# Optimization experiments

Hardware: AMD Instinct MI355X
Metric: run time of the kernel (lower is better)

The kernel has to match this reference:

```python
import jax, jax.numpy as jnp
import numpy as np

B, S, D, H = 1, 2048, 1024, 16
HD = D // H
S_SLOPE = 10.0      # soft_thres_layer s
C_MASK = -10000.0   # soft_thres_layer c == masked_bias
ALPHA = 0.0         # config.threshold
W_STD = 0.02        # GPT2 init std for weights


def setup_inputs() -> dict:
    key = jax.random.key(0)
    k1, k2, k3 = jax.random.split(key, 3)
    return {
        "hidden_states": jax.random.normal(k1, (B, S, D), dtype=jnp.float32),
        "c_attn_w": jax.random.normal(k2, (D, 3 * D), dtype=jnp.float32) * W_STD,
        "c_attn_b": jnp.zeros((3 * D,), dtype=jnp.float32),
        "c_proj_w": jax.random.normal(k3, (D, D), dtype=jnp.float32) * W_STD,
        "c_proj_b": jnp.zeros((D,), dtype=jnp.float32),
    }


def reference(hidden_states, c_attn_w, c_attn_b, c_proj_w, c_proj_b):
    # Conv1D: x @ w + b (GPT2 convention: weight is [in, out])
    qkv = hidden_states @ c_attn_w + c_attn_b            # [B,S,3D]
    q, k, v = jnp.split(qkv, 3, axis=-1)

    def split_heads(x):
        return x.reshape(B, S, H, HD).transpose(0, 2, 1, 3)  # [B,H,S,hd]

    q, k, v = split_heads(q), split_heads(k), split_heads(v)

    # prun path: NO 1/sqrt(d) scaling (skipped when self.prun is True)
    w = jnp.einsum("bhqd,bhkd->bhqk", q, k)              # [B,H,S,S]

    causal = jnp.tril(jnp.ones((S, S), dtype=bool))[None, None]
    w = jnp.where(causal, w, C_MASK)

    # soft-threshold pruning: smoothly pushes scores below alpha toward c=-10000
    w = C_MASK + (w - C_MASK) * jax.nn.sigmoid(S_SLOPE * (w - ALPHA))

    a = jax.nn.softmax(w, axis=-1)                        # attn_dropout = identity (eval)
    out = jnp.einsum("bhqk,bhkd->bhqd", a, v)             # [B,H,S,hd]
    out = out.transpose(0, 2, 1, 3).reshape(B, S, D)      # merge heads
    return out @ c_proj_w + c_proj_b                      # resid_dropout = identity
```

## Files before the change

kernel.cpp:

```cpp
#include <hip/hip_runtime.h>


#define S_LEN 2048
#define DM    1024
#define NH    16
#define HD    64
#define SLOPE 10.0f
#define CMASK -10000.0f
#define SP    2080

typedef short s16x4 __attribute__((ext_vector_type(4)));
typedef short s16x8 __attribute__((ext_vector_type(8)));
typedef float f32x4 __attribute__((ext_vector_type(4)));

#define MFMA16(a,b,c) __builtin_amdgcn_mfma_f32_16x16x32_bf16(a,b,c,0,0,0)
#define GLDS16(g,l) __builtin_amdgcn_global_load_lds( \
    (const __attribute__((address_space(1))) void*)(g), \
    (__attribute__((address_space(3))) void*)(l), 16, 0, 0)

__device__ __forceinline__ short f2bf(float f){
    unsigned u = __float_as_uint(f);
    u += 0x7fffu + ((u >> 16) & 1u);
    return (short)(u >> 16);
}
__device__ __forceinline__ float bf2f(short x){
    return __uint_as_float(((unsigned)(unsigned short)x) << 16);
}
struct bfpair { short hi, lo; };
__device__ __forceinline__ bfpair split_bf(float x){
    bfpair r; r.hi = f2bf(x);
    r.lo = f2bf(x - bf2f(r.hi));
    return r;
}

template<int ROWS, int THREADS>
__device__ __forceinline__ void stage_tile(const short* gbase, int rstride,
                                           short* lds, int tid){
#pragma unroll
    for (int it = 0; it < ROWS*8/THREADS; ++it){
        int s = it*THREADS + tid;
        int row = s >> 3, grp = s & 7;
        const short* src = gbase + (size_t)row*rstride + ((grp ^ (row & 7)) << 3);
        GLDS16(src, lds + (size_t)s*8);
    }
}
__device__ __forceinline__ s16x8 frag(const short* lds, int row, int kg){
    return *(const s16x8*)&lds[row*64 + ((kg ^ (row & 7)) << 3)];
}

__global__ __launch_bounds__(256)
void gemm_qkv(const short* __restrict__ Ahg, const short* __restrict__ Alg,
              const short* __restrict__ Bhg, const short* __restrict__ Blg,
              const float* __restrict__ bias,
              short* __restrict__ QHh, short* __restrict__ QHl,
              short* __restrict__ KH,  short* __restrict__ Vb)
{
    __shared__ __align__(16) short Ah_s[128*64];
    __shared__ __align__(16) short Bh_s[128*64];
    __shared__ __align__(16) short Al_s[128*64];
    __shared__ __align__(16) short Bl_s[128*64];

    const int tid = threadIdx.x, lane = tid & 63, wid = tid >> 6;
    const int lr = lane & 15, lg = lane >> 4;
    const int brow = blockIdx.y*128, bcol = blockIdx.x*128;
    const int sec = bcol >> 10;
    const int wm = (wid >> 1)*64, wn = (wid & 1)*64;

    f32x4 acc[4][4];
#pragma unroll
    for (int m = 0; m < 4; ++m)
#pragma unroll
        for (int n = 0; n < 4; ++n) acc[m][n] = (f32x4){0.f,0.f,0.f,0.f};

    for (int k0 = 0; k0 < DM; k0 += 64){
        stage_tile<128,256>(Ahg + (size_t)brow*DM + k0, DM, Ah_s, tid);
        stage_tile<128,256>(Bhg + (size_t)bcol*DM + k0, DM, Bh_s, tid);
        if (sec == 0){
            stage_tile<128,256>(Alg + (size_t)brow*DM + k0, DM, Al_s, tid);
            stage_tile<128,256>(Blg + (size_t)bcol*DM + k0, DM, Bl_s, tid);
        }
        __syncthreads();
#pragma unroll
        for (int kc = 0; kc < 2; ++kc){
            s16x8 ah[4], al[4], bh[4], bl[4];
#pragma unroll
            for (int m = 0; m < 4; ++m)
                ah[m] = frag(Ah_s, wm + m*16 + lr, kc*4 + lg);
#pragma unroll
            for (int n = 0; n < 4; ++n)
                bh[n] = frag(Bh_s, wn + n*16 + lr, kc*4 + lg);
            if (sec == 0){
#pragma unroll
                for (int m = 0; m < 4; ++m)
                    al[m] = frag(Al_s, wm + m*16 + lr, kc*4 + lg);
#pragma unroll
                for (int n = 0; n < 4; ++n)
                    bl[n] = frag(Bl_s, wn + n*16 + lr, kc*4 + lg);
            }
#pragma unroll
            for (int m = 0; m < 4; ++m)
#pragma unroll
                for (int n = 0; n < 4; ++n){
                    acc[m][n] = MFMA16(ah[m], bh[n], acc[m][n]);
                    if (sec == 0){
                        acc[m][n] = MFMA16(ah[m], bl[n], acc[m][n]);
                        acc[m][n] = MFMA16(al[m], bh[n], acc[m][n]);
                    }
                }
        }
        __syncthreads();
    }

#pragma unroll
    for (int m = 0; m < 4; ++m)
#pragma unroll
        for (int n = 0; n < 4; ++n){
            int row  = brow + wm + m*16 + lg*4;
            int gcol = bcol + wn + n*16 + lr;
            float bv = bias[gcol];
            int h0 = (gcol & 1023) >> 6, d = gcol & 63;
#pragma unroll
            for (int v = 0; v < 4; ++v){
                float val = acc[m][n][v] + bv;
                if (sec == 0){
                    bfpair p = split_bf(val);
                    size_t o = ((size_t)h0*S_LEN + row + v)*HD + d;
                    QHh[o] = p.hi; QHl[o] = p.lo;
                } else if (sec == 1){
                    KH[((size_t)h0*S_LEN + row + v)*HD + d] = f2bf(val);
                } else {
                    Vb[(size_t)(row + v)*DM + (gcol & 1023)] = f2bf(val);
                }
            }
        }
}

__global__ __launch_bounds__(256)
void gemm_proj(const short* __restrict__ Ahg, const short* __restrict__ Bhg,
               const float* __restrict__ bias, float* __restrict__ C)
{
    __shared__ __align__(16) short Ah_s[128*64];
    __shared__ __align__(16) short Bh_s[128*64];

    const int tid = threadIdx.x, lane = tid & 63, wid = tid >> 6;
    const int lr = lane & 15, lg = lane >> 4;
    const int brow = blockIdx.y*128, bcol = blockIdx.x*128;
    const int wm = (wid >> 1)*64, wn = (wid & 1)*64;

    f32x4 acc[4][4];
#pragma unroll
    for (int m = 0; m < 4; ++m)
#pragma unroll
        for (int n = 0; n < 4; ++n) acc[m][n] = (f32x4){0.f,0.f,0.f,0.f};

    for (int k0 = 0; k0 < DM; k0 += 64){
        stage_tile<128,256>(Ahg + (size_t)brow*DM + k0, DM, Ah_s, tid);
        stage_tile<128,256>(Bhg + (size_t)bcol*DM + k0, DM, Bh_s, tid);
        __syncthreads();
#pragma unroll
        for (int kc = 0; kc < 2; ++kc){
            s16x8 ah[4], bh[4];
#pragma unroll
            for (int m = 0; m < 4; ++m)
                ah[m] = frag(Ah_s, wm + m*16 + lr, kc*4 + lg);
#pragma unroll
            for (int n = 0; n < 4; ++n)
                bh[n] = frag(Bh_s, wn + n*16 + lr, kc*4 + lg);
#pragma unroll
            for (int m = 0; m < 4; ++m)
#pragma unroll
                for (int n = 0; n < 4; ++n)
                    acc[m][n] = MFMA16(ah[m], bh[n], acc[m][n]);
        }
        __syncthreads();
    }

#pragma unroll
    for (int m = 0; m < 4; ++m)
#pragma unroll
        for (int n = 0; n < 4; ++n){
            int row  = brow + wm + m*16 + lg*4;
            int gcol = bcol + wn + n*16 + lr;
            float bv = bias[gcol];
#pragma unroll
            for (int v = 0; v < 4; ++v)
                C[(size_t)(row + v)*DM + gcol] = acc[m][n][v] + bv;
        }
}

__global__ __launch_bounds__(256)
void split_f32(const float* __restrict__ x, short* __restrict__ h,
               short* __restrict__ l, int n4)
{
    int i = blockIdx.x*256 + threadIdx.x;
    if (i >= n4) return;
    float4 v = *(const float4*)&x[(size_t)i*4];
    bfpair a = split_bf(v.x), b = split_bf(v.y), c = split_bf(v.z), d = split_bf(v.w);
    s16x4 hv, lv;
    hv.x = a.hi; hv.y = b.hi; hv.z = c.hi; hv.w = d.hi;
    lv.x = a.lo; lv.y = b.lo; lv.z = c.lo; lv.w = d.lo;
    *(s16x4*)&h[(size_t)i*4] = hv;
    *(s16x4*)&l[(size_t)i*4] = lv;
}

template<bool SPL>
__global__ __launch_bounds__(256)
void wtrans(const float* __restrict__ W, int N, short* __restrict__ Th,
            short* __restrict__ Tl)
{
    __shared__ float t[64][65];
    const int tid = threadIdx.x;
    const int tn = blockIdx.x*64, tk = blockIdx.y*64;
#pragma unroll
    for (int it = 0; it < 4; ++it){
        int idx = tid + it*256;
        int r = idx >> 4, c4 = (idx & 15)*4;
        float4 v = *(const float4*)&W[(size_t)(tk + r)*N + tn + c4];
        t[r][c4] = v.x; t[r][c4+1] = v.y; t[r][c4+2] = v.z; t[r][c4+3] = v.w;
    }
    __syncthreads();
#pragma unroll
    for (int it = 0; it < 4; ++it){
        int idx = tid + it*256;
        int n = idx >> 4, c4 = (idx & 15)*4;
        s16x4 hv, lv;
#pragma unroll
        for (int j = 0; j < 4; ++j){
            bfpair p = split_bf(t[c4+j][n]);
            hv[j] = p.hi; lv[j] = p.lo;
        }
        *(s16x4*)&Th[(size_t)(tn + n)*DM + tk + c4] = hv;
        if (SPL && tn < DM)
            *(s16x4*)&Tl[(size_t)(tn + n)*DM + tk + c4] = lv;
    }
}

__global__ __launch_bounds__(256)
void vtrans(const short* __restrict__ Vb, short* __restrict__ Vt)
{
    __shared__ short t[64][66];
    const int tid = threadIdx.x;
    const int td = blockIdx.x*64, ts = blockIdx.y*64;
#pragma unroll
    for (int it = 0; it < 4; ++it){
        int idx = tid + it*256;
        int r = idx >> 4, c4 = (idx & 15)*4;
        s16x4 v = *(const s16x4*)&Vb[(size_t)(ts + r)*DM + td + c4];
        t[r][c4] = v.x; t[r][c4+1] = v.y; t[r][c4+2] = v.z; t[r][c4+3] = v.w;
    }
    __syncthreads();
#pragma unroll
    for (int it = 0; it < 4; ++it){
        int idx = tid + it*256;
        int n = idx >> 4, c4 = (idx & 15)*4;
        s16x4 o;
#pragma unroll
        for (int j = 0; j < 4; ++j) o[j] = t[c4+j][n];
        *(s16x4*)&Vt[(size_t)(td + n)*SP + ts + c4] = o;
    }
}

__global__ __launch_bounds__(64)
void sv_partial(const short* __restrict__ Vb, float* __restrict__ PB)
{
    int b = blockIdx.x, h = blockIdx.y, d = threadIdx.x;
    float s = 0.f;
#pragma unroll 8
    for (int k = 0; k < 64; ++k)
        s += bf2f(Vb[(size_t)(b*64 + k)*DM + h*HD + d]);
    PB[((size_t)h*32 + b)*64 + d] = s;
}
__global__ __launch_bounds__(64)
void sv_suffix(const float* __restrict__ PB, float* __restrict__ SSV)
{
    int h = blockIdx.x, d = threadIdx.x;
    float s = 0.f;
    SSV[((size_t)h*33 + 32)*64 + d] = 0.f;
    for (int b = 31; b >= 0; --b){
        s += PB[((size_t)h*32 + b)*64 + d];
        SSV[((size_t)h*33 + b)*64 + d] = s;
    }
}

__global__ __launch_bounds__(256)
void attn_fwd(const short* __restrict__ QHh, const short* __restrict__ QHl,
              const short* __restrict__ KH, const short* __restrict__ Vt,
              short* __restrict__ acc0, short* __restrict__ acc1,
              short* __restrict__ acc2, float* __restrict__ ML)
{
    __shared__ __align__(16) short kh_s[64*64];
    __shared__ __align__(16) short vt_s[64*64];
    __shared__ __align__(16) short Ps[4][16*72];

    const int j = blockIdx.x;
    const int h = (j & 7) + 8*((j >> 3) & 1);
    const int t = j >> 4;
    int qst, c;
    if (t < 8)      { qst = t; c = 0; }
    else if (t < 24){ int u = t - 8;  qst = 8  + (u >> 1); c = u & 1; }
    else if (t < 48){ int u = t - 24; qst = 16 + u/3;      c = u - (u/3)*3; }
    else            { int u = t - 48; qst = 24 + (u >> 2); c = u & 3; }
    const int kv0 = c*8;
    const int kv1 = min(kv0 + 8, qst + 1);

    const int tid = threadIdx.x, lane = tid & 63, wid = tid >> 6;
    const int lr = lane & 15, lg = lane >> 4;
    const int qrow = qst*64 + wid*16 + lg*4;

    const short* qbh = QHh + ((size_t)h*S_LEN + qst*64 + wid*16)*HD;
    const short* qbl = QHl + ((size_t)h*S_LEN + qst*64 + wid*16)*HD;
    s16x8 aqh[2], aql[2];
#pragma unroll
    for (int kc = 0; kc < 2; ++kc){
        aqh[kc] = *(const s16x8*)&qbh[lr*HD + kc*32 + lg*8];
        aql[kc] = *(const s16x8*)&qbl[lr*HD + kc*32 + lg*8];
    }

    float m_run[4], l_run[4];
    f32x4 acc_o[4];
#pragma unroll
    for (int v = 0; v < 4; ++v){ m_run[v] = -1e30f; l_run[v] = 0.f; }
#pragma unroll
    for (int n = 0; n < 4; ++n) acc_o[n] = (f32x4){0.f,0.f,0.f,0.f};

    for (int kvb = kv0; kvb < kv1; ++kvb){
        __syncthreads();
        stage_tile<64,256>(KH + ((size_t)h*S_LEN + kvb*64)*HD, HD, kh_s, tid);
        stage_tile<64,256>(Vt + (size_t)(h*HD)*SP + kvb*64, SP, vt_s, tid);
        __syncthreads();

        f32x4 sc[4];
#pragma unroll
        for (int n = 0; n < 4; ++n) sc[n] = (f32x4){0.f,0.f,0.f,0.f};
#pragma unroll
        for (int kc = 0; kc < 2; ++kc)
#pragma unroll
            for (int n = 0; n < 4; ++n){
                s16x8 bkh = frag(kh_s, n*16 + lr, kc*4 + lg);
                sc[n] = MFMA16(aqh[kc], bkh, sc[n]);
                sc[n] = MFMA16(aql[kc], bkh, sc[n]);
            }

        float p[4][4], tmax[4];
#pragma unroll
        for (int v = 0; v < 4; ++v) tmax[v] = -1e30f;
        if (kvb == qst){
#pragma unroll
            for (int n = 0; n < 4; ++n){
                int key = kvb*64 + n*16 + lr;
#pragma unroll
                for (int v = 0; v < 4; ++v){
                    float w;
                    if (key > qrow + v) w = CMASK;
                    else {
                        float sv = sc[n][v];
                        float sig = 1.f / (1.f + __expf(-SLOPE*sv));
                        w = CMASK + (sv - CMASK)*sig;
                    }
                    p[n][v] = w;
                    tmax[v] = fmaxf(tmax[v], w);
                }
            }
        } else {
#pragma unroll
            for (int n = 0; n < 4; ++n)
#pragma unroll
                for (int v = 0; v < 4; ++v){
                    float sv = sc[n][v];
                    float sig = 1.f / (1.f + __expf(-SLOPE*sv));
                    float w = CMASK + (sv - CMASK)*sig;
                    p[n][v] = w;
                    tmax[v] = fmaxf(tmax[v], w);
                }
        }
#pragma unroll
        for (int v = 0; v < 4; ++v)
#pragma unroll
            for (int msk = 1; msk < 16; msk <<= 1)
                tmax[v] = fmaxf(tmax[v], __shfl_xor(tmax[v], msk, 64));

        float scale[4], rsum[4];
#pragma unroll
        for (int v = 0; v < 4; ++v){
            float mn = fmaxf(m_run[v], tmax[v]);
            scale[v] = __expf(m_run[v] - mn);
            m_run[v] = mn;
            rsum[v] = 0.f;
        }
#pragma unroll
        for (int n = 0; n < 4; ++n)
#pragma unroll
            for (int v = 0; v < 4; ++v){
                float e = __expf(p[n][v] - m_run[v]);
                p[n][v] = e;
                rsum[v] += e;
            }
#pragma unroll
        for (int v = 0; v < 4; ++v){
#pragma unroll
            for (int msk = 1; msk < 16; msk <<= 1)
                rsum[v] += __shfl_xor(rsum[v], msk, 64);
            l_run[v] = l_run[v]*scale[v] + rsum[v];
        }
#pragma unroll
        for (int n = 0; n < 4; ++n)
#pragma unroll
            for (int v = 0; v < 4; ++v) acc_o[n][v] *= scale[v];

#pragma unroll
        for (int n = 0; n < 4; ++n)
#pragma unroll
            for (int v = 0; v < 4; ++v)
                Ps[wid][(lg*4 + v)*72 + 16*n + lr] = f2bf(p[n][v]);
        asm volatile("s_waitcnt lgkmcnt(0)" ::: "memory");

        s16x8 pa0 = *(const s16x8*)&Ps[wid][lr*72 + lg*8];
        s16x8 pa1 = *(const s16x8*)&Ps[wid][lr*72 + 32 + lg*8];
#pragma unroll
        for (int n = 0; n < 4; ++n){
            s16x8 bv0 = frag(vt_s, 16*n + lr, lg);
            s16x8 bv1 = frag(vt_s, 16*n + lr, 4 + lg);
            acc_o[n] = MFMA16(pa0, bv0, acc_o[n]);
            acc_o[n] = MFMA16(pa1, bv1, acc_o[n]);
        }
    }

    short* ab = (j < 512) ? acc0 + (size_t)j*4096
              : (j < 768) ? acc1 + (size_t)(j-512)*4096
                          : acc2 + (size_t)(j-768)*4096;
#pragma unroll
    for (int n = 0; n < 4; ++n)
#pragma unroll
        for (int v = 0; v < 4; ++v)
            ab[(wid*16 + lg*4 + v)*64 + 16*n + lr] = f2bf(acc_o[n][v]);
    if (lr == 0){
#pragma unroll
        for (int v = 0; v < 4; ++v){
            ML[((size_t)j*64 + wid*16 + lg*4 + v)*2 + 0] = m_run[v];
            ML[((size_t)j*64 + wid*16 + lg*4 + v)*2 + 1] = l_run[v];
        }
    }
}

__global__ __launch_bounds__(256)
void attn_merge(const short* __restrict__ acc0, const short* __restrict__ acc1,
                const short* __restrict__ acc2, const float* __restrict__ ML,
                const float* __restrict__ SSV, short* __restrict__ O)
{
    const int b = blockIdx.x;
    const int h = b & 15, qst = b >> 4;
    const int d = threadIdx.x & 63, rg = threadIdx.x >> 6;
    const int C = (qst + 8) >> 3;
    const int tbase = (qst < 8)  ? qst
                    : (qst < 16) ? 8  + 2*(qst - 8)
                    : (qst < 24) ? 24 + 3*(qst - 16)
                                 : 48 + 4*(qst - 24);
    const float F = (float)(S_LEN - 64*(qst + 1));
    const float svd = SSV[((size_t)h*33 + (qst + 1))*64 + d];

    for (int i = 0; i < 16; ++i){
        int r = rg + 4*i;
        float M = -1e30f;
        for (int c = 0; c < C; ++c){
            int job = (tbase + c)*16 + h;
            M = fmaxf(M, ML[((size_t)job*64 + r)*2]);
        }
        float num = 0.f, den = 0.f;
        for (int c = 0; c < C; ++c){
            int job = (tbase + c)*16 + h;
            float m = ML[((size_t)job*64 + r)*2];
            float l = ML[((size_t)job*64 + r)*2 + 1];
            const short* ab = (job < 512) ? acc0 + (size_t)job*4096
                            : (job < 768) ? acc1 + (size_t)(job-512)*4096
                                          : acc2 + (size_t)(job-768)*4096;
            float e = __expf(m - M);
            num += e * bf2f(ab[r*64 + d]);
            den += e * l;
        }
        float et = __expf(CMASK - M);
        num += et * svd;
        den += et * F;
        O[(size_t)(qst*64 + r)*DM + h*64 + d] = f2bf(num/den);
    }
}

extern "C" void kernel_launch(void* const* d_in, const int* in_sizes, int n_in,
                              void* d_out, int out_size, void* d_ws, size_t ws_size,
                              hipStream_t stream)
{
    (void)in_sizes; (void)n_in; (void)out_size; (void)ws_size;
    const float* hs   = (const float*)d_in[0];
    const float* wqkv = (const float*)d_in[1];
    const float* bqkv = (const float*)d_in[2];
    const float* wprj = (const float*)d_in[3];
    const float* bprj = (const float*)d_in[4];

    char* p = (char*)d_ws;
    short* Ahg  = (short*)(p + (0ull  << 20));
    short* Alg  = (short*)(p + (4ull  << 20));
    short* WqTh = (short*)(p + (8ull  << 20));
    short* WqTl = (short*)(p + (14ull << 20));
    short* QHh  = (short*)(p + (16ull << 20));
    short* QHl  = (short*)(p + (20ull << 20));
    short* KH   = (short*)(p + (24ull << 20));
    short* Vbg  = (short*)(p + (28ull << 20));
    short* VT   = (short*)(p + (32ull << 20));
    float* PB   = (float*)(p + (38ull << 20));
    float* SSV  = (float*)(p + (38ull << 20) + (256ull << 10));
    float* ML   = (float*)(p + (39ull << 20));
    short* O    = Ahg;
    short* WpT  = WqTh;

    split_f32<<<S_LEN*DM/4/256, 256, 0, stream>>>(hs, Ahg, Alg, S_LEN*DM/4);
    wtrans<true><<<dim3(3*DM/64, DM/64), 256, 0, stream>>>(wqkv, 3*DM, WqTh, WqTl);

    gemm_qkv<<<dim3(24, 16), 256, 0, stream>>>(
        Ahg, Alg, WqTh, WqTl, bqkv, QHh, QHl, KH, Vbg);

    wtrans<false><<<dim3(DM/64, DM/64), 256, 0, stream>>>(wprj, DM, WpT, nullptr);
    vtrans<<<dim3(DM/64, S_LEN/64), 256, 0, stream>>>(Vbg, VT);
    sv_partial<<<dim3(32, NH), 64, 0, stream>>>(Vbg, PB);
    sv_suffix<<<NH, 64, 0, stream>>>(PB, SSV);

    attn_fwd<<<1280, 256, 0, stream>>>(QHh, QHl, KH, VT, Alg, WqTl, Vbg, ML);
    attn_merge<<<512, 256, 0, stream>>>(Alg, WqTl, Vbg, ML, SSV, O);

    gemm_proj<<<dim3(8, 16), 256, 0, stream>>>(O, WpT, bprj, (float*)d_out);
}
```

Before: 181.6 us.

## Fuse prep kernels, fold split-bf16 Q GEMM into K=3072 loop, merge sv_partial into vtrans

Merges the input split and both weight transposes into one prep kernel, so the hi/lo parts sit side by side and the Q-section GEMM becomes a single K=3072 loop instead of three MFMAs per step with a branch. The Q/K/V column blocks are interleaved across blockIdx.x to balance load, and the V column sums are folded into the vtrans kernel, which drops the sv_partial launch. The soft-threshold now uses a cheaper rearranged form that clamps to CMASK below -1.5, and the merge division becomes a fast reciprocal. The workspace layout and the accumulator buffer indexing are reshuffled to match. The clamp and the fast division add small numeric differences.

```diff
diff --git a/kernel.cpp b/kernel.cpp
--- a/kernel.cpp
+++ b/kernel.cpp
@@ -33,6 +33,12 @@
     return r;
 }
 
+__device__ __forceinline__ float softthr(float sv){
+    float E = __expf(-SLOPE*sv);
+    float w = sv - __fdividef((sv - CMASK)*E, 1.f + E);
+    return (sv > -1.5f) ? w : CMASK;
+}
+
 template<int ROWS, int THREADS>
 __device__ __forceinline__ void stage_tile(const short* gbase, int rstride,
                                            short* lds, int tid){
@@ -49,168 +55,33 @@
 }
 
 __global__ __launch_bounds__(256)
-void gemm_qkv(const short* __restrict__ Ahg, const short* __restrict__ Alg,
-              const short* __restrict__ Bhg, const short* __restrict__ Blg,
-              const float* __restrict__ bias,
-              short* __restrict__ QHh, short* __restrict__ QHl,
-              short* __restrict__ KH,  short* __restrict__ Vb)
-{
-    __shared__ __align__(16) short Ah_s[128*64];
-    __shared__ __align__(16) short Bh_s[128*64];
-    __shared__ __align__(16) short Al_s[128*64];
-    __shared__ __align__(16) short Bl_s[128*64];
-
-    const int tid = threadIdx.x, lane = tid & 63, wid = tid >> 6;
-    const int lr = lane & 15, lg = lane >> 4;
-    const int brow = blockIdx.y*128, bcol = blockIdx.x*128;
-    const int sec = bcol >> 10;
-    const int wm = (wid >> 1)*64, wn = (wid & 1)*64;
-
-    f32x4 acc[4][4];
-#pragma unroll
-    for (int m = 0; m < 4; ++m)
-#pragma unroll
-        for (int n = 0; n < 4; ++n) acc[m][n] = (f32x4){0.f,0.f,0.f,0.f};
-
-    for (int k0 = 0; k0 < DM; k0 += 64){
-        stage_tile<128,256>(Ahg + (size_t)brow*DM + k0, DM, Ah_s, tid);
-        stage_tile<128,256>(Bhg + (size_t)bcol*DM + k0, DM, Bh_s, tid);
-        if (sec == 0){
-            stage_tile<128,256>(Alg + (size_t)brow*DM + k0, DM, Al_s, tid);
-            stage_tile<128,256>(Blg + (size_t)bcol*DM + k0, DM, Bl_s, tid);
-        }
-        __syncthreads();
-#pragma unroll
-        for (int kc = 0; kc < 2; ++kc){
-            s16x8 ah[4], al[4], bh[4], bl[4];
-#pragma unroll
-            for (int m = 0; m < 4; ++m)
-                ah[m] = frag(Ah_s, wm + m*16 + lr, kc*4 + lg);
-#pragma unroll
-            for (int n = 0; n < 4; ++n)
-                bh[n] = frag(Bh_s, wn + n*16 + lr, kc*4 + lg);
-            if (sec == 0){
-#pragma unroll
-                for (int m = 0; m < 4; ++m)
-                    al[m] = frag(Al_s, wm + m*16 + lr, kc*4 + lg);
-#pragma unroll
-                for (int n = 0; n < 4; ++n)
-                    bl[n] = frag(Bl_s, wn + n*16 + lr, kc*4 + lg);
-            }
-#pragma unroll
-            for (int m = 0; m < 4; ++m)
-#pragma unroll
-                for (int n = 0; n < 4; ++n){
-                    acc[m][n] = MFMA16(ah[m], bh[n], acc[m][n]);
-                    if (sec == 0){
-                        acc[m][n] = MFMA16(ah[m], bl[n], acc[m][n]);
-                        acc[m][n] = MFMA16(al[m], bh[n], acc[m][n]);
-                    }
-                }
-        }
-        __syncthreads();
-    }
-
-#pragma unroll
-    for (int m = 0; m < 4; ++m)
-#pragma unroll
-        for (int n = 0; n < 4; ++n){
-            int row  = brow + wm + m*16 + lg*4;
-            int gcol = bcol + wn + n*16 + lr;
-            float bv = bias[gcol];
-            int h0 = (gcol & 1023) >> 6, d = gcol & 63;
-#pragma unroll
-            for (int v = 0; v < 4; ++v){
-                float val = acc[m][n][v] + bv;
-                if (sec == 0){
-                    bfpair p = split_bf(val);
-                    size_t o = ((size_t)h0*S_LEN + row + v)*HD + d;
-                    QHh[o] = p.hi; QHl[o] = p.lo;
-                } else if (sec == 1){
-                    KH[((size_t)h0*S_LEN + row + v)*HD + d] = f2bf(val);
-                } else {
-                    Vb[(size_t)(row + v)*DM + (gcol & 1023)] = f2bf(val);
-                }
-            }
-        }
-}
-
-__global__ __launch_bounds__(256)
-void gemm_proj(const short* __restrict__ Ahg, const short* __restrict__ Bhg,
-               const float* __restrict__ bias, float* __restrict__ C)
-{
-    __shared__ __align__(16) short Ah_s[128*64];
-    __shared__ __align__(16) short Bh_s[128*64];
-
-    const int tid = threadIdx.x, lane = tid & 63, wid = tid >> 6;
-    const int lr = lane & 15, lg = lane >> 4;
-    const int brow = blockIdx.y*128, bcol = blockIdx.x*128;
-    const int wm = (wid >> 1)*64, wn = (wid & 1)*64;
-
-    f32x4 acc[4][4];
-#pragma unroll
-    for (int m = 0; m < 4; ++m)
-#pragma unroll
-        for (int n = 0; n < 4; ++n) acc[m][n] = (f32x4){0.f,0.f,0.f,0.f};
-
-    for (int k0 = 0; k0 < DM; k0 += 64){
-        stage_tile<128,256>(Ahg + (size_t)brow*DM + k0, DM, Ah_s, tid);
-        stage_tile<128,256>(Bhg + (size_t)bcol*DM + k0, DM, Bh_s, tid);
-        __syncthreads();
-#pragma unroll
-        for (int kc = 0; kc < 2; ++kc){
-            s16x8 ah[4], bh[4];
-#pragma unroll
-            for (int m = 0; m < 4; ++m)
-                ah[m] = frag(Ah_s, wm + m*16 + lr, kc*4 + lg);
-#pragma unroll
-            for (int n = 0; n < 4; ++n)
-                bh[n] = frag(Bh_s, wn + n*16 + lr, kc*4 + lg);
-#pragma unroll
-            for (int m = 0; m < 4; ++m)
-#pragma unroll
-                for (int n = 0; n < 4; ++n)
-                    acc[m][n] = MFMA16(ah[m], bh[n], acc[m][n]);
-        }
-        __syncthreads();
-    }
-
-#pragma unroll
-    for (int m = 0; m < 4; ++m)
-#pragma unroll
-        for (int n = 0; n < 4; ++n){
-            int row  = brow + wm + m*16 + lg*4;
-            int gcol = bcol + wn + n*16 + lr;
-            float bv = bias[gcol];
-#pragma unroll
-            for (int v = 0; v < 4; ++v)
-                C[(size_t)(row + v)*DM + gcol] = acc[m][n][v] + bv;
-        }
-}
-
-__global__ __launch_bounds__(256)
-void split_f32(const float* __restrict__ x, short* __restrict__ h,
-               short* __restrict__ l, int n4)
-{
-    int i = blockIdx.x*256 + threadIdx.x;
-    if (i >= n4) return;
-    float4 v = *(const float4*)&x[(size_t)i*4];
-    bfpair a = split_bf(v.x), b = split_bf(v.y), c = split_bf(v.z), d = split_bf(v.w);
-    s16x4 hv, lv;
-    hv.x = a.hi; hv.y = b.hi; hv.z = c.hi; hv.w = d.hi;
-    lv.x = a.lo; lv.y = b.lo; lv.z = c.lo; lv.w = d.lo;
-    *(s16x4*)&h[(size_t)i*4] = hv;
-    *(s16x4*)&l[(size_t)i*4] = lv;
-}
-
-template<bool SPL>
-__global__ __launch_bounds__(256)
-void wtrans(const float* __restrict__ W, int N, short* __restrict__ Th,
-            short* __restrict__ Tl)
+void prep(const float* __restrict__ hs, const float* __restrict__ wqkv,
+          const float* __restrict__ wprj, short* __restrict__ Ahl,
+          short* __restrict__ WqT, short* __restrict__ WkvT,
+          short* __restrict__ WpT)
 {
     __shared__ float t[64][65];
-    const int tid = threadIdx.x;
-    const int tn = blockIdx.x*64, tk = blockIdx.y*64;
+    const int bx = blockIdx.x, tid = threadIdx.x;
+
+    if (bx < 2048){
+        int i = bx*256 + tid;
+        int elem = i*4, row = elem >> 10, col = elem & 1023;
+        float4 v = *(const float4*)&hs[(size_t)elem];
+        bfpair a = split_bf(v.x), b = split_bf(v.y), c = split_bf(v.z), d = split_bf(v.w);
+        s16x4 hv, lv;
+        hv.x = a.hi; hv.y = b.hi; hv.z = c.hi; hv.w = d.hi;
+        lv.x = a.lo; lv.y = b.lo; lv.z = c.lo; lv.w = d.lo;
+        *(s16x4*)&Ahl[(size_t)row*2048 + col] = hv;
+        *(s16x4*)&Ahl[(size_t)row*2048 + 1024 + col] = lv;
+        return;
+    }
+
+    const float* W; int N, u;
+    if (bx < 2816){ u = bx - 2048; W = wqkv; N = 3072; }
+    else          { u = bx - 2816; W = wprj; N = 1024; }
+    const int ntiles = N >> 6;
+    const int tn = (u % ntiles)*64, tk = (u / ntiles)*64;
+
 #pragma unroll
     for (int it = 0; it < 4; ++it){
         int idx = tid + it*256;
@@ -229,18 +100,154 @@
             bfpair p = split_bf(t[c4+j][n]);
             hv[j] = p.hi; lv[j] = p.lo;
         }
-        *(s16x4*)&Th[(size_t)(tn + n)*DM + tk + c4] = hv;
-        if (SPL && tn < DM)
-            *(s16x4*)&Tl[(size_t)(tn + n)*DM + tk + c4] = lv;
+        if (bx >= 2816){
+            *(s16x4*)&WpT[(size_t)(tn + n)*1024 + tk + c4] = hv;
+        } else if (tn < 1024){
+            *(s16x4*)&WqT[(size_t)(tn + n)*2048 + tk + c4] = hv;
+            *(s16x4*)&WqT[(size_t)(tn + n)*2048 + 1024 + tk + c4] = lv;
+        } else {
+            *(s16x4*)&WkvT[(size_t)(tn + n - 1024)*1024 + tk + c4] = hv;
+        }
     }
 }
 
 __global__ __launch_bounds__(256)
-void vtrans(const short* __restrict__ Vb, short* __restrict__ Vt)
+void gemm_qkv(const short* __restrict__ Ahl, const short* __restrict__ WqT,
+              const short* __restrict__ WkvT, const float* __restrict__ bias,
+              short* __restrict__ QHh, short* __restrict__ QHl,
+              short* __restrict__ KH,  short* __restrict__ Vb)
+{
+    __shared__ __align__(16) short Ah_s[128*64];
+    __shared__ __align__(16) short Bh_s[128*64];
+
+    const int tid = threadIdx.x, lane = tid & 63, wid = tid >> 6;
+    const int lr = lane & 15, lg = lane >> 4;
+    const int brow = blockIdx.y*128;
+    const int xs = blockIdx.x % 3, xi = blockIdx.x / 3;
+    const int bcol = xs*1024 + xi*128;
+    const bool isQ = (xs == 0);
+    const int KTOT = isQ ? 3072 : 1024;
+    const short* Bbase = isQ ? (WqT + (size_t)bcol*2048)
+                             : (WkvT + (size_t)(bcol - 1024)*1024);
+    const int bstride = isQ ? 2048 : 1024;
+    const int wm = (wid >> 1)*64, wn = (wid & 1)*64;
+
+    f32x4 acc[4][4];
+#pragma unroll
+    for (int m = 0; m < 4; ++m)
+#pragma unroll
+        for (int n = 0; n < 4; ++n) acc[m][n] = (f32x4){0.f,0.f,0.f,0.f};
+
+    for (int k0 = 0; k0 < KTOT; k0 += 64){
+        int acol  = (k0 < 2048) ? k0 : k0 - 2048;
+        int bcolk = (isQ && k0 >= 1024) ? k0 - 1024 : k0;
+        stage_tile<128,256>(Ahl + (size_t)brow*2048 + acol, 2048, Ah_s, tid);
+        stage_tile<128,256>(Bbase + bcolk, bstride, Bh_s, tid);
+        __syncthreads();
+#pragma unroll
+        for (int kc = 0; kc < 2; ++kc){
+            s16x8 ah[4], bh[4];
+#pragma unroll
+            for (int m = 0; m < 4; ++m)
+                ah[m] = frag(Ah_s, wm + m*16 + lr, kc*4 + lg);
+#pragma unroll
+            for (int n = 0; n < 4; ++n)
+                bh[n] = frag(Bh_s, wn + n*16 + lr, kc*4 + lg);
+#pragma unroll
+            for (int m = 0; m < 4; ++m)
+#pragma unroll
+                for (int n = 0; n < 4; ++n)
+                    acc[m][n] = MFMA16(ah[m], bh[n], acc[m][n]);
+        }
+        __syncthreads();
+    }
+
+#pragma unroll
+    for (int m = 0; m < 4; ++m)
+#pragma unroll
+        for (int n = 0; n < 4; ++n){
+            int row  = brow + wm + m*16 + lg*4;
+            int gcol = bcol + wn + n*16 + lr;
+            float bv = bias[gcol];
+            int col1 = gcol & 1023;
+            int h0 = col1 >> 6, d = col1 & 63;
+#pragma unroll
+            for (int v = 0; v < 4; ++v){
+                float val = acc[m][n][v] + bv;
+                if (xs == 0){
+                    bfpair p = split_bf(val);
+                    size_t o = ((size_t)h0*S_LEN + row + v)*HD + d;
+                    QHh[o] = p.hi; QHl[o] = p.lo;
+                } else if (xs == 1){
+                    KH[((size_t)h0*S_LEN + row + v)*HD + d] = f2bf(val);
+                } else {
+                    Vb[(size_t)(row + v)*DM + col1] = f2bf(val);
+                }
+            }
+        }
+}
+
+__global__ __launch_bounds__(256)
+void gemm_proj(const short* __restrict__ Ahg, const short* __restrict__ Bhg,
+               const float* __restrict__ bias, float* __restrict__ C)
+{
+    __shared__ __align__(16) short Ah_s[128*64];
+    __shared__ __align__(16) short Bh_s[128*64];
+
+    const int tid = threadIdx.x, lane = tid & 63, wid = tid >> 6;
+    const int lr = lane & 15, lg = lane >> 4;
+    const int brow = blockIdx.y*128, bcol = blockIdx.x*128;
+    const int wm = (wid >> 1)*64, wn = (wid & 1)*64;
+
+    f32x4 acc[4][4];
+#pragma unroll
+    for (int m = 0; m < 4; ++m)
+#pragma unroll
+        for (int n = 0; n < 4; ++n) acc[m][n] = (f32x4){0.f,0.f,0.f,0.f};
+
+    for (int k0 = 0; k0 < DM; k0 += 64){
+        stage_tile<128,256>(Ahg + (size_t)brow*DM + k0, DM, Ah_s, tid);
+        stage_tile<128,256>(Bhg + (size_t)bcol*DM + k0, DM, Bh_s, tid);
+        __syncthreads();
+#pragma unroll
+        for (int kc = 0; kc < 2; ++kc){
+            s16x8 ah[4], bh[4];
+#pragma unroll
+            for (int m = 0; m < 4; ++m)
+                ah[m] = frag(Ah_s, wm + m*16 + lr, kc*4 + lg);
+#pragma unroll
+            for (int n = 0; n < 4; ++n)
+                bh[n] = frag(Bh_s, wn + n*16 + lr, kc*4 + lg);
+#pragma unroll
+            for (int m = 0; m < 4; ++m)
+#pragma unroll
+                for (int n = 0; n < 4; ++n)
+                    acc[m][n] = MFMA16(ah[m], bh[n], acc[m][n]);
+        }
+        __syncthreads();
+    }
+
+#pragma unroll
+    for (int m = 0; m < 4; ++m)
+#pragma unroll
+        for (int n = 0; n < 4; ++n){
+            int row  = brow + wm + m*16 + lg*4;
+            int gcol = bcol + wn + n*16 + lr;
+            float bv = bias[gcol];
+#pragma unroll
+            for (int v = 0; v < 4; ++v)
+                C[(size_t)(row + v)*DM + gcol] = acc[m][n][v] + bv;
+        }
+}
+
+__global__ __launch_bounds__(256)
+void vtrans(const short* __restrict__ Vb, short* __restrict__ Vt,
+            float* __restrict__ PB)
 {
     __shared__ short t[64][66];
     const int tid = threadIdx.x;
-    const int td = blockIdx.x*64, ts = blockIdx.y*64;
+    const int h = blockIdx.x, b = blockIdx.y;
+    const int td = h*64, ts = b*64;
 #pragma unroll
     for (int it = 0; it < 4; ++it){
         int idx = tid + it*256;
@@ -258,18 +265,14 @@
         for (int j = 0; j < 4; ++j) o[j] = t[c4+j][n];
         *(s16x4*)&Vt[(size_t)(td + n)*SP + ts + c4] = o;
     }
-}
-
-__global__ __launch_bounds__(64)
-void sv_partial(const short* __restrict__ Vb, float* __restrict__ PB)
-{
-    int b = blockIdx.x, h = blockIdx.y, d = threadIdx.x;
-    float s = 0.f;
+    if (tid < 64){
+        float s = 0.f;
 #pragma unroll 8
-    for (int k = 0; k < 64; ++k)
-        s += bf2f(Vb[(size_t)(b*64 + k)*DM + h*HD + d]);
-    PB[((size_t)h*32 + b)*64 + d] = s;
-}
+        for (int r = 0; r < 64; ++r) s += bf2f(t[r][tid]);
+        PB[((size_t)h*32 + b)*64 + tid] = s;
+    }
+}
+
 __global__ __launch_bounds__(64)
 void sv_suffix(const float* __restrict__ PB, float* __restrict__ SSV)
 {
@@ -350,13 +353,7 @@
                 int key = kvb*64 + n*16 + lr;
 #pragma unroll
                 for (int v = 0; v < 4; ++v){
-                    float w;
-                    if (key > qrow + v) w = CMASK;
-                    else {
-                        float sv = sc[n][v];
-                        float sig = 1.f / (1.f + __expf(-SLOPE*sv));
-                        w = CMASK + (sv - CMASK)*sig;
-                    }
+                    float w = (key > qrow + v) ? CMASK : softthr(sc[n][v]);
                     p[n][v] = w;
                     tmax[v] = fmaxf(tmax[v], w);
                 }
@@ -366,9 +363,7 @@
             for (int n = 0; n < 4; ++n)
 #pragma unroll
                 for (int v = 0; v < 4; ++v){
-                    float sv = sc[n][v];
-                    float sig = 1.f / (1.f + __expf(-SLOPE*sv));
-                    float w = CMASK + (sv - CMASK)*sig;
+                    float w = softthr(sc[n][v]);
                     p[n][v] = w;
                     tmax[v] = fmaxf(tmax[v], w);
                 }
@@ -425,9 +420,9 @@
         }
     }
 
-    short* ab = (j < 512) ? acc0 + (size_t)j*4096
-              : (j < 768) ? acc1 + (size_t)(j-512)*4096
-                          : acc2 + (size_t)(j-768)*4096;
+    short* ab = (j < 512)  ? acc0 + (size_t)j*4096
+              : (j < 1024) ? acc1 + (size_t)(j-512)*4096
+                           : acc2 + (size_t)(j-1024)*4096;
 #pragma unroll
     for (int n = 0; n < 4; ++n)
 #pragma unroll
@@ -470,9 +465,9 @@
             int job = (tbase + c)*16 + h;
             float m = ML[((size_t)job*64 + r)*2];
             float l = ML[((size_t)job*64 + r)*2 + 1];
-            const short* ab = (job < 512) ? acc0 + (size_t)job*4096
-                            : (job < 768) ? acc1 + (size_t)(job-512)*4096
-                                          : acc2 + (size_t)(job-768)*4096;
+            const short* ab = (job < 512)  ? acc0 + (size_t)job*4096
+                            : (job < 1024) ? acc1 + (size_t)(job-512)*4096
+                                           : acc2 + (size_t)(job-1024)*4096;
             float e = __expf(m - M);
             num += e * bf2f(ab[r*64 + d]);
             den += e * l;
@@ -480,7 +475,7 @@
         float et = __expf(CMASK - M);
         num += et * svd;
         den += et * F;
-        O[(size_t)(qst*64 + r)*DM + h*64 + d] = f2bf(num/den);
+        O[(size_t)(qst*64 + r)*DM + h*64 + d] = f2bf(num * __fdividef(1.f, den));
     }
 }
 
@@ -496,34 +491,33 @@
     const float* bprj = (const float*)d_in[4];
 
     char* p = (char*)d_ws;
-    short* Ahg  = (short*)(p + (0ull  << 20));
-    short* Alg  = (short*)(p + (4ull  << 20));
-    short* WqTh = (short*)(p + (8ull  << 20));
-    short* WqTl = (short*)(p + (14ull << 20));
-    short* QHh  = (short*)(p + (16ull << 20));
-    short* QHl  = (short*)(p + (20ull << 20));
-    short* KH   = (short*)(p + (24ull << 20));
-    short* Vbg  = (short*)(p + (28ull << 20));
-    short* VT   = (short*)(p + (32ull << 20));
-    float* PB   = (float*)(p + (38ull << 20));
-    float* SSV  = (float*)(p + (38ull << 20) + (256ull << 10));
-    float* ML   = (float*)(p + (39ull << 20));
-    short* O    = Ahg;
-    short* WpT  = WqTh;
-
-    split_f32<<<S_LEN*DM/4/256, 256, 0, stream>>>(hs, Ahg, Alg, S_LEN*DM/4);
-    wtrans<true><<<dim3(3*DM/64, DM/64), 256, 0, stream>>>(wqkv, 3*DM, WqTh, WqTl);
+    short* Ahl  = (short*)(p + (0ull  << 20));
+    short* WqT  = (short*)(p + (8ull  << 20));
+    short* WkvT = (short*)(p + (12ull << 20));
+    short* WpT  = (short*)(p + (16ull << 20));
+    short* QHh  = (short*)(p + (18ull << 20));
+    short* QHl  = (short*)(p + (22ull << 20));
+    short* KH   = (short*)(p + (26ull << 20));
+    short* Vbg  = (short*)(p + (30ull << 20));
+    short* VT   = (short*)(p + (34ull << 20));
+    float* PB   = (float*)(p + (38ull << 20) + (256ull << 10));
+    float* SSV  = (float*)(p + (38ull << 20) + (512ull << 10));
+    short* O    = Ahl;
+    short* accA = (short*)(p + (4ull  << 20));
+    short* accB = (short*)(p + (8ull  << 20));
+    short* accC = (short*)(p + (12ull << 20));
+    float* ML   = (float*)(p + (14ull << 20));
+
+    prep<<<3072, 256, 0, stream>>>(hs, wqkv, wprj, Ahl, WqT, WkvT, WpT);
 
     gemm_qkv<<<dim3(24, 16), 256, 0, stream>>>(
-        Ahg, Alg, WqTh, WqTl, bqkv, QHh, QHl, KH, Vbg);
-
-    wtrans<false><<<dim3(DM/64, DM/64), 256, 0, stream>>>(wprj, DM, WpT, nullptr);
-    vtrans<<<dim3(DM/64, S_LEN/64), 256, 0, stream>>>(Vbg, VT);
-    sv_partial<<<dim3(32, NH), 64, 0, stream>>>(Vbg, PB);
+        Ahl, WqT, WkvT, bqkv, QHh, QHl, KH, Vbg);
+
+    vtrans<<<dim3(NH, S_LEN/64), 256, 0, stream>>>(Vbg, VT, PB);
     sv_suffix<<<NH, 64, 0, stream>>>(PB, SSV);
 
-    attn_fwd<<<1280, 256, 0, stream>>>(QHh, QHl, KH, VT, Alg, WqTl, Vbg, ML);
-    attn_merge<<<512, 256, 0, stream>>>(Alg, WqTl, Vbg, ML, SSV, O);
+    attn_fwd<<<1280, 256, 0, stream>>>(QHh, QHl, KH, VT, accA, accB, accC, ML);
+    attn_merge<<<512, 256, 0, stream>>>(accA, accB, accC, ML, SSV, O);
 
     gemm_proj<<<dim3(8, 16), 256, 0, stream>>>(O, WpT, bprj, (float*)d_out);
 }
```

New measurement: 195.6 us. 1.08x slower.
